# Performance work log

Measured on AMD Instinct MI355X. Metric: run time of the kernel, lower is better.

## Reference

```python
import jax, jax.numpy as jnp
import numpy as np

WIN = 7  # skimage structural_similarity default win_size


def _uniform_valid(x):
    # x: [N, H, W] -> [N, H-6, W-6]; 7x7 uniform (box) filter, VALID.
    # exactly equivalent to uniform_filter + crop (boundary mode irrelevant).
    k = jnp.ones((1, 1, WIN, WIN), x.dtype) / (WIN * WIN)
    y = jax.lax.conv_general_dilated(x[:, None], k, (1, 1), 'VALID')
    return y[:, 0]


def _ssim_frames(x, y):
    # K1=0.01, K2=0.03, data_range=255, sample covariance (N/(N-1)).
    C1 = (0.01 * 255.0) ** 2
    C2 = (0.03 * 255.0) ** 2
    NP = WIN * WIN
    cov_norm = NP / (NP - 1.0)
    ux = _uniform_valid(x)
    uy = _uniform_valid(y)
    uxx = _uniform_valid(x * x)
    uyy = _uniform_valid(y * y)
    uxy = _uniform_valid(x * y)
    vx = cov_norm * (uxx - ux * ux)
    vy = cov_norm * (uyy - uy * uy)
    vxy = cov_norm * (uxy - ux * uy)
    S = ((2.0 * ux * uy + C1) * (2.0 * vxy + C2)) / (
        (ux * ux + uy * uy + C1) * (vx + vy + C2))
    return jnp.mean(S, axis=(1, 2))  # per-frame mean SSIM


def setup_inputs() -> dict:
    key = jax.random.key(0)
    k1, k2, k3 = jax.random.split(key, 3)
    B, T, C, H, W = 8, 20, 1, 512, 512
    gen_img = jax.random.uniform(k1, (B, T, C, H, W), dtype=jnp.float32)
    target = jax.random.uniform(k2, (B, T, C, H, W), dtype=jnp.float32)
    gen_D = jax.random.normal(k3, (B, 1), dtype=jnp.float32)
    return {"gen_img": gen_img, "target": target, "gen_D": gen_D}


def reference(gen_img, target, gen_D):
    B, T, C, H, W = gen_img.shape
    diff = gen_img - target
    L_rec = jnp.mean(jnp.abs(diff)) + jnp.mean(diff * diff)
    # SSIM on channel 0 of every frame, scaled by 255 (as in the numpy loop);
    # original detaches, so stop_gradient for faithfulness.
    x = gen_img[:, :, 0].reshape(B * T, H, W) * 255.0
    y = target[:, :, 0].reshape(B * T, H, W) * 255.0
    L_ssim = jnp.mean(jax.lax.stop_gradient(_ssim_frames(x, y)))
    L_adv = -jnp.mean(gen_D)
    L_total = L_rec + 0.01 * (1.0 - L_ssim) + 0.0001 * L_adv
    return (L_total, L_rec, L_ssim, L_adv)
```

## Files before the change

kernel.cpp:

```cpp
#include <hip/hip_runtime.h>

#define FRAMES 160
#define HH 512
#define WW 512
#define STRIPS 16
#define NBLK (STRIPS * FRAMES)
#define NTOT 41943040

__device__ __forceinline__ float ssim_fast(float a, float b, float sxx,
                                           float syy, float sxy) {
  const float K1 = 0.2401f;
  const float K2 = 2.1609f;
  const float cA = 49.0f / 24.0f;
  const float cB = 49.0f / 48.0f;
  float ab = a * b;
  float s2 = fmaf(a, a, b * b);
  float A1 = fmaf(2.0f, ab, K1);
  float B1 = s2 + K1;
  float A2 = fmaf(cA, fmaf(49.0f, sxy, -ab), K2);
  float B2 = fmaf(cB, fmaf(49.0f, sxx + syy, -s2), K2);
  return (A1 * A2) * __builtin_amdgcn_rcpf(B1 * B2);
}

#define HSTORE(S, P, A)                          \
  P.x = S.x; P.y = P.x + S.y;                    \
  P.z = P.y + S.z; P.w = P.z + S.w;              \
  lds[grp][A][0][q] = make_float2(P.x, P.y);     \
  lds[grp][A][1][q] = make_float2(P.z, P.w);

#define HWIN(P, W, A) {                          \
  float2 h1 = lds[grp][A][1][q + 1];             \
  float2 l2 = lds[grp][A][0][q + 2];             \
  W.x = P.w + h1.x;                              \
  W.y = (P.w - P.x) + h1.y;                      \
  W.z = (P.w - P.y) + (h1.y + l2.x);             \
  W.w = (P.w - P.z) + (h1.y + l2.y); }

#define LREC(xv, yv) {                                         \
  float4 d_ = make_float4(xv.x - yv.x, xv.y - yv.y,            \
                          xv.z - yv.z, xv.w - yv.w);           \
  sabs += fabsf(d_.x) + fabsf(d_.y) + fabsf(d_.z) + fabsf(d_.w); \
  ssq += d_.x * d_.x + d_.y * d_.y;                            \
  ssq += d_.z * d_.z + d_.w * d_.w; }

#define VADD(xv, yv)                                    \
  Sx += xv; Sy += yv;                                   \
  Sxx += xv * xv; Syy += yv * yv; Sxy += xv * yv;

#define VSUB(xv, yv)                                    \
  Sx -= xv; Sy -= yv;                                   \
  Sxx -= xv * xv; Syy -= yv * yv; Sxy -= xv * yv;

__global__ __launch_bounds__(256) void fused_kernel(
    const float* __restrict__ gsrc, const float* __restrict__ tsrc,
    float* __restrict__ ws) {
  const int strip = blockIdx.x;
  const int frame = blockIdx.y;
  const int row0 = strip * 32;
  const int n_iter = (strip == STRIPS - 1) ? 13 : 16;
  const int tid = threadIdx.x;
  const int grp = tid >> 7;
  const int q = tid & 127;

  const float* gp = gsrc + ((size_t)frame * HH + row0 + grp) * WW + q * 4;
  const float* tp = tsrc + ((size_t)frame * HH + row0 + grp) * WW + q * 4;

  __shared__ float2 lds[2][5][2][132];

  float4 Sx = make_float4(0.f, 0.f, 0.f, 0.f);
  float4 Sy = Sx, Sxx = Sx, Syy = Sx, Sxy = Sx;
  float sabs = 0.f, ssq = 0.f, ssum = 0.f;

  for (int i = 0; i < 7; ++i) {
    float4 xv = *(const float4*)(gp + i * WW);
    float4 yv = *(const float4*)(tp + i * WW);
    VADD(xv, yv)
    if (grp == 0) { LREC(xv, yv) }
  }

  for (int it = 0; it < n_iter; ++it) {
    float4 Px, Py, Pxx, Pyy, Pxy;
    HSTORE(Sx, Px, 0) HSTORE(Sy, Py, 1) HSTORE(Sxx, Pxx, 2)
    HSTORE(Syy, Pyy, 3) HSTORE(Sxy, Pxy, 4)
    __syncthreads();
    float4 Wx, Wy, Wxx, Wyy, Wxy;
    HWIN(Px, Wx, 0) HWIN(Py, Wy, 1) HWIN(Pxx, Wxx, 2)
    HWIN(Pyy, Wyy, 3) HWIN(Pxy, Wxy, 4)
    float v0 = ssim_fast(Wx.x, Wy.x, Wxx.x, Wyy.x, Wxy.x);
    float v1 = ssim_fast(Wx.y, Wy.y, Wxx.y, Wyy.y, Wxy.y);
    float v2 = ssim_fast(Wx.z, Wy.z, Wxx.z, Wyy.z, Wxy.z);
    float v3 = ssim_fast(Wx.w, Wy.w, Wxx.w, Wyy.w, Wxy.w);
    ssum += (q <= 126) ? v0 : 0.f;
    ssum += (q <= 126) ? v1 : 0.f;
    ssum += (q <= 125) ? v2 : 0.f;
    ssum += (q <= 125) ? v3 : 0.f;
    __syncthreads();

    if (it + 1 < n_iter) {
      const float* pn = gp + (size_t)(2 * it + 7) * WW;
      const float* qn = tp + (size_t)(2 * it + 7) * WW;
      const float* po = gp + (size_t)(2 * it) * WW;
      const float* qo = tp + (size_t)(2 * it) * WW;
      {
        float4 nx = *(const float4*)pn;
        float4 ny = *(const float4*)qn;
        float4 ox = *(const float4*)po;
        float4 oy = *(const float4*)qo;
        VADD(nx, ny)
        VSUB(ox, oy)
        if ((grp == 0) && (2 * it + 7 <= 30)) { LREC(nx, ny) }
      }
      {
        float4 nx = *(const float4*)(pn + WW);
        float4 ny = *(const float4*)(qn + WW);
        float4 ox = *(const float4*)(po + WW);
        float4 oy = *(const float4*)(qo + WW);
        VADD(nx, ny)
        VSUB(ox, oy)
        bool cnt = (grp == 0) ? (2 * it + 8 <= 30) : (2 * it + 9 == 31);
        if (cnt) { LREC(nx, ny) }
      }
    }
  }

  #pragma unroll
  for (int off = 32; off > 0; off >>= 1) {
    sabs += __shfl_down(sabs, off, 64);
    ssq += __shfl_down(ssq, off, 64);
    ssum += __shfl_down(ssum, off, 64);
  }
  float* scr = (float*)&lds[0][0][0][0];
  const int lane = tid & 63, wv = tid >> 6;
  if (lane == 0) { scr[wv] = sabs; scr[4 + wv] = ssq; scr[8 + wv] = ssum; }
  __syncthreads();
  if (tid == 0) {
    const int bid = blockIdx.y * STRIPS + blockIdx.x;
    ws[bid] = scr[0] + scr[1] + scr[2] + scr[3];
    ws[NBLK + bid] = scr[4] + scr[5] + scr[6] + scr[7];
    ws[2 * NBLK + bid] = scr[8] + scr[9] + scr[10] + scr[11];
  }
}

__global__ __launch_bounds__(256) void finalize_kernel(
    const float* __restrict__ ws, const float* __restrict__ genD,
    float* __restrict__ out) {
  const int tid = threadIdx.x;
  float a = 0.f, b = 0.f, c = 0.f;
  for (int i = tid; i < NBLK; i += 256) {
    a += ws[i];
    b += ws[NBLK + i];
    c += ws[2 * NBLK + i];
  }
  #pragma unroll
  for (int off = 32; off > 0; off >>= 1) {
    a += __shfl_down(a, off, 64);
    b += __shfl_down(b, off, 64);
    c += __shfl_down(c, off, 64);
  }
  __shared__ float la[4], lb[4], lc[4];
  const int lane = tid & 63, wv = tid >> 6;
  if (lane == 0) { la[wv] = a; lb[wv] = b; lc[wv] = c; }
  __syncthreads();
  if (tid == 0) {
    a = la[0] + la[1] + la[2] + la[3];
    b = lb[0] + lb[1] + lb[2] + lb[3];
    c = lc[0] + lc[1] + lc[2] + lc[3];
    const float invN = 1.0f / (float)NTOT;
    float L_rec = a * invN + b * invN;
    float L_ssim = c / (160.0f * 506.0f * 506.0f);
    float d = 0.f;
    #pragma unroll
    for (int i = 0; i < 8; ++i) d += genD[i];
    float L_adv = -d / 8.0f;
    float L_total = L_rec + 0.01f * (1.0f - L_ssim) + 0.0001f * L_adv;
    out[0] = L_total;
    out[1] = L_rec;
    out[2] = L_ssim;
    out[3] = L_adv;
  }
}

extern "C" void kernel_launch(void* const* d_in, const int* in_sizes, int n_in,
                              void* d_out, int out_size, void* d_ws,
                              size_t ws_size, hipStream_t stream) {
  const float* gen_img = (const float*)d_in[0];
  const float* target = (const float*)d_in[1];
  const float* gen_D = (const float*)d_in[2];
  float* out = (float*)d_out;
  float* ws = (float*)d_ws;

  dim3 grid(STRIPS, FRAMES);
  fused_kernel<<<grid, 256, 0, stream>>>(gen_img, target, ws);
  finalize_kernel<<<1, 256, 0, stream>>>(ws, gen_D, out);
}
```

Measured before the change: 375.9 us.

## Prefetch next-row global loads before LDS phase and use lgkm-only barriers

```diff
diff --git a/kernel.cpp b/kernel.cpp
--- a/kernel.cpp
+++ b/kernel.cpp
@@ -6,6 +6,11 @@
 #define STRIPS 16
 #define NBLK (STRIPS * FRAMES)
 #define NTOT 41943040
+
+__device__ __forceinline__ void sync_lds() {
+  __builtin_amdgcn_s_waitcnt(0xC07F);
+  __builtin_amdgcn_s_barrier();
+}
 
 __device__ __forceinline__ float ssim_fast(float a, float b, float sxx,
                                            float syy, float sxy) {
@@ -51,7 +56,7 @@
   Sx -= xv; Sy -= yv;                                   \
   Sxx -= xv * xv; Syy -= yv * yv; Sxy -= xv * yv;
 
-__global__ __launch_bounds__(256) void fused_kernel(
+__global__ __launch_bounds__(256, 4) void fused_kernel(
     const float* __restrict__ gsrc, const float* __restrict__ tsrc,
     float* __restrict__ ws) {
   const int strip = blockIdx.x;
@@ -79,10 +84,27 @@
   }
 
   for (int it = 0; it < n_iter; ++it) {
+    const bool slide = (it + 1 < n_iter);
+    float4 nx0, ny0, nx1, ny1, ox0, oy0, ox1, oy1;
+    if (slide) {
+      const float* pn = gp + (size_t)(2 * it + 7) * WW;
+      const float* qn = tp + (size_t)(2 * it + 7) * WW;
+      const float* po = gp + (size_t)(2 * it) * WW;
+      const float* qo = tp + (size_t)(2 * it) * WW;
+      nx0 = *(const float4*)pn;
+      ny0 = *(const float4*)qn;
+      nx1 = *(const float4*)(pn + WW);
+      ny1 = *(const float4*)(qn + WW);
+      ox0 = *(const float4*)po;
+      oy0 = *(const float4*)qo;
+      ox1 = *(const float4*)(po + WW);
+      oy1 = *(const float4*)(qo + WW);
+    }
+
     float4 Px, Py, Pxx, Pyy, Pxy;
     HSTORE(Sx, Px, 0) HSTORE(Sy, Py, 1) HSTORE(Sxx, Pxx, 2)
     HSTORE(Syy, Pyy, 3) HSTORE(Sxy, Pxy, 4)
-    __syncthreads();
+    sync_lds();
     float4 Wx, Wy, Wxx, Wyy, Wxy;
     HWIN(Px, Wx, 0) HWIN(Py, Wy, 1) HWIN(Pxx, Wxx, 2)
     HWIN(Pyy, Wyy, 3) HWIN(Pxy, Wxy, 4)
@@ -94,32 +116,16 @@
     ssum += (q <= 126) ? v1 : 0.f;
     ssum += (q <= 125) ? v2 : 0.f;
     ssum += (q <= 125) ? v3 : 0.f;
-    __syncthreads();
-
-    if (it + 1 < n_iter) {
-      const float* pn = gp + (size_t)(2 * it + 7) * WW;
-      const float* qn = tp + (size_t)(2 * it + 7) * WW;
-      const float* po = gp + (size_t)(2 * it) * WW;
-      const float* qo = tp + (size_t)(2 * it) * WW;
-      {
-        float4 nx = *(const float4*)pn;
-        float4 ny = *(const float4*)qn;
-        float4 ox = *(const float4*)po;
-        float4 oy = *(const float4*)qo;
-        VADD(nx, ny)
-        VSUB(ox, oy)
-        if ((grp == 0) && (2 * it + 7 <= 30)) { LREC(nx, ny) }
-      }
-      {
-        float4 nx = *(const float4*)(pn + WW);
-        float4 ny = *(const float4*)(qn + WW);
-        float4 ox = *(const float4*)(po + WW);
-        float4 oy = *(const float4*)(qo + WW);
-        VADD(nx, ny)
-        VSUB(ox, oy)
-        bool cnt = (grp == 0) ? (2 * it + 8 <= 30) : (2 * it + 9 == 31);
-        if (cnt) { LREC(nx, ny) }
-      }
+    sync_lds();
+
+    if (slide) {
+      VADD(nx0, ny0)
+      VSUB(ox0, oy0)
+      if ((grp == 0) && (2 * it + 7 <= 30)) { LREC(nx0, ny0) }
+      VADD(nx1, ny1)
+      VSUB(ox1, oy1)
+      bool cnt = (grp == 0) ? (2 * it + 8 <= 30) : (2 * it + 9 == 31);
+      if (cnt) { LREC(nx1, ny1) }
     }
   }
 
@@ -129,6 +135,7 @@
     ssq += __shfl_down(ssq, off, 64);
     ssum += __shfl_down(ssum, off, 64);
   }
+  __syncthreads();
   float* scr = (float*)&lds[0][0][0][0];
   const int lane = tid & 63, wv = tid >> 6;
   if (lane == 0) { scr[wv] = sabs; scr[4 + wv] = ssq; scr[8 + wv] = ssum; }
```

New measurement: 355.5 us. -5.4%, faster.

## Use single-wave blocks with 8 columns per lane and shuffle-based horizontal box sums

Applied to the files above, without the earlier changes.

```diff
diff --git a/kernel.cpp b/kernel.cpp
--- a/kernel.cpp
+++ b/kernel.cpp
@@ -3,12 +3,12 @@
 #define FRAMES 160
 #define HH 512
 #define WW 512
-#define STRIPS 16
-#define NBLK (STRIPS * FRAMES)
+#define WSTRIPS 16
+#define NW (WSTRIPS * FRAMES)
 #define NTOT 41943040
 
-__device__ __forceinline__ float ssim_fast(float a, float b, float sxx,
-                                           float syy, float sxy) {
+__device__ __forceinline__ float ssim_fast(float a, float b, float szz,
+                                           float sxy) {
   const float K1 = 0.2401f;
   const float K2 = 2.1609f;
   const float cA = 49.0f / 24.0f;
@@ -18,107 +18,122 @@
   float A1 = fmaf(2.0f, ab, K1);
   float B1 = s2 + K1;
   float A2 = fmaf(cA, fmaf(49.0f, sxy, -ab), K2);
-  float B2 = fmaf(cB, fmaf(49.0f, sxx + syy, -s2), K2);
+  float B2 = fmaf(cB, fmaf(49.0f, szz, -s2), K2);
   return (A1 * A2) * __builtin_amdgcn_rcpf(B1 * B2);
 }
 
-#define HSTORE(S, P, A)                          \
-  P.x = S.x; P.y = P.x + S.y;                    \
-  P.z = P.y + S.z; P.w = P.z + S.w;              \
-  lds[grp][A][0][q] = make_float2(P.x, P.y);     \
-  lds[grp][A][1][q] = make_float2(P.z, P.w);
-
-#define HWIN(P, W, A) {                          \
-  float2 h1 = lds[grp][A][1][q + 1];             \
-  float2 l2 = lds[grp][A][0][q + 2];             \
-  W.x = P.w + h1.x;                              \
-  W.y = (P.w - P.x) + h1.y;                      \
-  W.z = (P.w - P.y) + (h1.y + l2.x);             \
-  W.w = (P.w - P.z) + (h1.y + l2.y); }
-
-#define LREC(xv, yv) {                                         \
-  float4 d_ = make_float4(xv.x - yv.x, xv.y - yv.y,            \
-                          xv.z - yv.z, xv.w - yv.w);           \
-  sabs += fabsf(d_.x) + fabsf(d_.y) + fabsf(d_.z) + fabsf(d_.w); \
-  ssq += d_.x * d_.x + d_.y * d_.y;                            \
-  ssq += d_.z * d_.z + d_.w * d_.w; }
-
-#define VADD(xv, yv)                                    \
-  Sx += xv; Sy += yv;                                   \
-  Sxx += xv * xv; Syy += yv * yv; Sxy += xv * yv;
-
-#define VSUB(xv, yv)                                    \
-  Sx -= xv; Sy -= yv;                                   \
-  Sxx -= xv * xv; Syy -= yv * yv; Sxy -= xv * yv;
-
-__global__ __launch_bounds__(256) void fused_kernel(
+#define LOAD8(dst, ptr) {                         \
+  float4 lo_ = *(const float4*)(ptr);             \
+  float4 hi_ = *(const float4*)((ptr) + 4);       \
+  dst[0] = lo_.x; dst[1] = lo_.y;                 \
+  dst[2] = lo_.z; dst[3] = lo_.w;                 \
+  dst[4] = hi_.x; dst[5] = hi_.y;                 \
+  dst[6] = hi_.z; dst[7] = hi_.w; }
+
+__global__ __launch_bounds__(64) void fused_kernel(
     const float* __restrict__ gsrc, const float* __restrict__ tsrc,
     float* __restrict__ ws) {
-  const int strip = blockIdx.x;
-  const int frame = blockIdx.y;
+  const int frame = blockIdx.x;
+  const int strip = blockIdx.y;
   const int row0 = strip * 32;
-  const int n_iter = (strip == STRIPS - 1) ? 13 : 16;
-  const int tid = threadIdx.x;
-  const int grp = tid >> 7;
-  const int q = tid & 127;
-
-  const float* gp = gsrc + ((size_t)frame * HH + row0 + grp) * WW + q * 4;
-  const float* tp = tsrc + ((size_t)frame * HH + row0 + grp) * WW + q * 4;
-
-  __shared__ float2 lds[2][5][2][132];
-
-  float4 Sx = make_float4(0.f, 0.f, 0.f, 0.f);
-  float4 Sy = Sx, Sxx = Sx, Syy = Sx, Sxy = Sx;
+  const int R = (strip == WSTRIPS - 1) ? 26 : 32;
+  const int lane = threadIdx.x;
+
+  const float* gp = gsrc + ((size_t)frame * HH + row0) * WW + lane * 8;
+  const float* tp = tsrc + ((size_t)frame * HH + row0) * WW + lane * 8;
+
+  float sx[8], sy[8], szz[8], sxy[8];
+  #pragma unroll
+  for (int k = 0; k < 8; ++k) {
+    sx[k] = 0.f; sy[k] = 0.f; szz[k] = 0.f; sxy[k] = 0.f;
+  }
   float sabs = 0.f, ssq = 0.f, ssum = 0.f;
 
-  for (int i = 0; i < 7; ++i) {
-    float4 xv = *(const float4*)(gp + i * WW);
-    float4 yv = *(const float4*)(tp + i * WW);
-    VADD(xv, yv)
-    if (grp == 0) { LREC(xv, yv) }
-  }
-
-  for (int it = 0; it < n_iter; ++it) {
-    float4 Px, Py, Pxx, Pyy, Pxy;
-    HSTORE(Sx, Px, 0) HSTORE(Sy, Py, 1) HSTORE(Sxx, Pxx, 2)
-    HSTORE(Syy, Pyy, 3) HSTORE(Sxy, Pxy, 4)
-    __syncthreads();
-    float4 Wx, Wy, Wxx, Wyy, Wxy;
-    HWIN(Px, Wx, 0) HWIN(Py, Wy, 1) HWIN(Pxx, Wxx, 2)
-    HWIN(Pyy, Wyy, 3) HWIN(Pxy, Wxy, 4)
-    float v0 = ssim_fast(Wx.x, Wy.x, Wxx.x, Wyy.x, Wxy.x);
-    float v1 = ssim_fast(Wx.y, Wy.y, Wxx.y, Wyy.y, Wxy.y);
-    float v2 = ssim_fast(Wx.z, Wy.z, Wxx.z, Wyy.z, Wxy.z);
-    float v3 = ssim_fast(Wx.w, Wy.w, Wxx.w, Wyy.w, Wxy.w);
-    ssum += (q <= 126) ? v0 : 0.f;
-    ssum += (q <= 126) ? v1 : 0.f;
-    ssum += (q <= 125) ? v2 : 0.f;
-    ssum += (q <= 125) ? v3 : 0.f;
-    __syncthreads();
-
-    if (it + 1 < n_iter) {
-      const float* pn = gp + (size_t)(2 * it + 7) * WW;
-      const float* qn = tp + (size_t)(2 * it + 7) * WW;
-      const float* po = gp + (size_t)(2 * it) * WW;
-      const float* qo = tp + (size_t)(2 * it) * WW;
-      {
-        float4 nx = *(const float4*)pn;
-        float4 ny = *(const float4*)qn;
-        float4 ox = *(const float4*)po;
-        float4 oy = *(const float4*)qo;
-        VADD(nx, ny)
-        VSUB(ox, oy)
-        if ((grp == 0) && (2 * it + 7 <= 30)) { LREC(nx, ny) }
+  #pragma unroll
+  for (int i = 0; i < 6; ++i) {
+    float xv[8], yv[8];
+    LOAD8(xv, gp + i * WW)
+    LOAD8(yv, tp + i * WW)
+    #pragma unroll
+    for (int k = 0; k < 8; ++k) {
+      sx[k] += xv[k];
+      sy[k] += yv[k];
+      szz[k] = fmaf(xv[k], xv[k], szz[k]);
+      szz[k] = fmaf(yv[k], yv[k], szz[k]);
+      sxy[k] = fmaf(xv[k], yv[k], sxy[k]);
+      float d = xv[k] - yv[k];
+      sabs += fabsf(d);
+      ssq = fmaf(d, d, ssq);
+    }
+  }
+
+  for (int r = 0; r < R; ++r) {
+    float nx[8], ny[8];
+    LOAD8(nx, gp + (r + 6) * WW)
+    LOAD8(ny, tp + (r + 6) * WW)
+    const bool ret = (r + 1 < R);
+    float ox[8], oy[8];
+    if (ret) {
+      LOAD8(ox, gp + r * WW)
+      LOAD8(oy, tp + r * WW)
+    }
+
+    #pragma unroll
+    for (int k = 0; k < 8; ++k) {
+      sx[k] += nx[k];
+      sy[k] += ny[k];
+      szz[k] = fmaf(nx[k], nx[k], szz[k]);
+      szz[k] = fmaf(ny[k], ny[k], szz[k]);
+      sxy[k] = fmaf(nx[k], ny[k], sxy[k]);
+    }
+    if (r <= 25) {
+      #pragma unroll
+      for (int k = 0; k < 8; ++k) {
+        float d = nx[k] - ny[k];
+        sabs += fabsf(d);
+        ssq = fmaf(d, d, ssq);
       }
-      {
-        float4 nx = *(const float4*)(pn + WW);
-        float4 ny = *(const float4*)(qn + WW);
-        float4 ox = *(const float4*)(po + WW);
-        float4 oy = *(const float4*)(qo + WW);
-        VADD(nx, ny)
-        VSUB(ox, oy)
-        bool cnt = (grp == 0) ? (2 * it + 8 <= 30) : (2 * it + 9 == 31);
-        if (cnt) { LREC(nx, ny) }
+    }
+
+    float px[8], py[8], pz[8], pq[8];
+    px[0] = sx[0]; py[0] = sy[0]; pz[0] = szz[0]; pq[0] = sxy[0];
+    #pragma unroll
+    for (int k = 1; k < 8; ++k) {
+      px[k] = px[k - 1] + sx[k];
+      py[k] = py[k - 1] + sy[k];
+      pz[k] = pz[k - 1] + szz[k];
+      pq[k] = pq[k - 1] + sxy[k];
+    }
+    float nxp[6], nyp[6], nzp[6], nqp[6];
+    #pragma unroll
+    for (int k = 0; k < 6; ++k) {
+      nxp[k] = __shfl_down(px[k], 1, 64);
+      nyp[k] = __shfl_down(py[k], 1, 64);
+      nzp[k] = __shfl_down(pz[k], 1, 64);
+      nqp[k] = __shfl_down(pq[k], 1, 64);
+    }
+
+    ssum += ssim_fast(px[6], py[6], pz[6], pq[6]);
+    ssum += ssim_fast(px[7] - px[0], py[7] - py[0], pz[7] - pz[0],
+                      pq[7] - pq[0]);
+    #pragma unroll
+    for (int j = 2; j < 8; ++j) {
+      float wx = (px[7] - px[j - 1]) + nxp[j - 2];
+      float wy = (py[7] - py[j - 1]) + nyp[j - 2];
+      float wz = (pz[7] - pz[j - 1]) + nzp[j - 2];
+      float wq = (pq[7] - pq[j - 1]) + nqp[j - 2];
+      float v = ssim_fast(wx, wy, wz, wq);
+      ssum += (lane < 63) ? v : 0.f;
+    }
+
+    if (ret) {
+      #pragma unroll
+      for (int k = 0; k < 8; ++k) {
+        sx[k] -= ox[k];
+        sy[k] -= oy[k];
+        szz[k] = fmaf(-ox[k], ox[k], szz[k]);
+        szz[k] = fmaf(-oy[k], oy[k], szz[k]);
+        sxy[k] = fmaf(-ox[k], oy[k], sxy[k]);
       }
     }
   }
@@ -129,15 +144,11 @@
     ssq += __shfl_down(ssq, off, 64);
     ssum += __shfl_down(ssum, off, 64);
   }
-  float* scr = (float*)&lds[0][0][0][0];
-  const int lane = tid & 63, wv = tid >> 6;
-  if (lane == 0) { scr[wv] = sabs; scr[4 + wv] = ssq; scr[8 + wv] = ssum; }
-  __syncthreads();
-  if (tid == 0) {
-    const int bid = blockIdx.y * STRIPS + blockIdx.x;
-    ws[bid] = scr[0] + scr[1] + scr[2] + scr[3];
-    ws[NBLK + bid] = scr[4] + scr[5] + scr[6] + scr[7];
-    ws[2 * NBLK + bid] = scr[8] + scr[9] + scr[10] + scr[11];
+  if (lane == 0) {
+    const int wid = strip * FRAMES + frame;
+    ws[wid] = sabs;
+    ws[NW + wid] = ssq;
+    ws[2 * NW + wid] = ssum;
   }
 }
 
@@ -146,10 +157,10 @@
     float* __restrict__ out) {
   const int tid = threadIdx.x;
   float a = 0.f, b = 0.f, c = 0.f;
-  for (int i = tid; i < NBLK; i += 256) {
+  for (int i = tid; i < NW; i += 256) {
     a += ws[i];
-    b += ws[NBLK + i];
-    c += ws[2 * NBLK + i];
+    b += ws[NW + i];
+    c += ws[2 * NW + i];
   }
   #pragma unroll
   for (int off = 32; off > 0; off >>= 1) {
@@ -189,7 +200,7 @@
   float* out = (float*)d_out;
   float* ws = (float*)d_ws;
 
-  dim3 grid(STRIPS, FRAMES);
-  fused_kernel<<<grid, 256, 0, stream>>>(gen_img, target, ws);
+  dim3 grid(FRAMES, WSTRIPS);
+  fused_kernel<<<grid, 64, 0, stream>>>(gen_img, target, ws);
   finalize_kernel<<<1, 256, 0, stream>>>(ws, gen_D, out);
 }
```

Result: no change. 369.5 us (-1.7%).
